# Performance work log

Measured on AMD Instinct MI355X. Metric: run time of the kernel, lower is better.

## Reference

```python
import jax, jax.numpy as jnp
import numpy as np

T, H, I, E, K = 4096, 2048, 1408, 8, 2


def setup_inputs() -> dict:
    key = jax.random.key(0)
    k1, k2, k3, k4, k5 = jax.random.split(key, 5)
    hidden_states = jax.random.normal(k1, (T, H), dtype=jnp.float32)
    w13 = jax.random.normal(k2, (E, 2 * I, H), dtype=jnp.float32) * 0.02
    w2 = jax.random.normal(k3, (E, H, I), dtype=jnp.float32) * 0.02
    topk_ids = jax.random.randint(k4, (T, K), 0, E, dtype=jnp.int32)
    topk_weights = jax.random.uniform(k5, (T, K), dtype=jnp.float32)
    return {
        "hidden_states": hidden_states,
        "w13": w13,
        "w2": w2,
        "topk_ids": topk_ids,
        "topk_weights": topk_weights,
    }


def reference(hidden_states, w13, w2, topk_ids, topk_weights):
    # hidden_states: [T, H]; w13: [E, 2I, H]; w2: [E, H, I]
    # topk_ids/topk_weights: [T, K]. local_expert_start = 0.
    num_tokens, hidden = hidden_states.shape
    num_experts = w13.shape[0]
    inter = w13.shape[1] // 2
    gate_w = w13[:, :inter, :]  # [E, I, H]
    up_w = w13[:, inter:, :]    # [E, I, H]

    # Dense per-expert gate/up projections (vectorized grouped GEMM).
    gate = jnp.einsum('th,eih->tei', hidden_states, gate_w)
    up = jnp.einsum('th,eih->tei', hidden_states, up_w)
    act = jax.nn.silu(gate) * up  # [T, E, I]

    # Scatter topk weights into a dense [T, E] routing matrix (zero elsewhere),
    # which reproduces the trivial impl's per-slot weighted accumulation.
    tok = jnp.arange(num_tokens, dtype=jnp.int32)[:, None]
    routing = jnp.zeros((num_tokens, num_experts), dtype=hidden_states.dtype)
    routing = routing.at[tok, topk_ids].add(topk_weights)

    # Weighted combine through the down projection; weighting act first avoids
    # materializing a [T, E, H] intermediate.
    act_w = act * routing[:, :, None]  # [T, E, I]
    out = jnp.einsum('tei,ehi->th', act_w, w2)  # [T, H]
    return out
```

## Files before the change

### kernel.cpp

```cpp
#include <hip/hip_runtime.h>
#include <hip/hip_bf16.h>

#define T_TOK 4096
#define HID   2048
#define INTER 1408
#define TWO_I 2816
#define NEXP  8
#define ROWCAP 9216

#define N8_HS  1048576
#define N8_W13 5767168
#define NCVT   ((N8_HS + N8_W13) / 256)

using bf16x8 = __attribute__((ext_vector_type(8))) __bf16;
using f32x4  = __attribute__((ext_vector_type(4))) float;

__device__ __forceinline__ unsigned short f2bf(float f) {
  unsigned u = __float_as_uint(f);
  u += 0x7fffu + ((u >> 16) & 1u);
  return (unsigned short)(u >> 16);
}

__device__ __forceinline__ void gload16(const void* g, void* l) {
  __builtin_amdgcn_global_load_lds(
      (const __attribute__((address_space(1))) void*)g,
      (__attribute__((address_space(3))) void*)l, 16, 0, 0);
}

__device__ __forceinline__ uint4 pack8(float4 a, float4 b) {
  union { unsigned short us[8]; uint4 v; } o;
  o.us[0] = f2bf(a.x); o.us[1] = f2bf(a.y); o.us[2] = f2bf(a.z); o.us[3] = f2bf(a.w);
  o.us[4] = f2bf(b.x); o.us[5] = f2bf(b.y); o.us[6] = f2bf(b.z); o.us[7] = f2bf(b.w);
  return o.v;
}

__global__ void cvt2route_kernel(const float* __restrict__ hs_f, unsigned short* __restrict__ hs_b,
                                 const float* __restrict__ w13_f, unsigned short* __restrict__ w13_b,
                                 const int* __restrict__ ids, const float* __restrict__ wts,
                                 float* __restrict__ R, int* __restrict__ counts) {
  int bid = blockIdx.x;
  if (bid >= NCVT) {
    int t = (bid - NCVT) * 256 + threadIdx.x;
    if (t >= T_TOK) return;
    int e0 = ids[t * 2], e1 = ids[t * 2 + 1];
    float w0 = wts[t * 2], w1 = wts[t * 2 + 1];
#pragma unroll
    for (int ee = 0; ee < NEXP; ++ee) {
      float r = (e0 == ee ? w0 : 0.0f) + (e1 == ee ? w1 : 0.0f);
      R[t * NEXP + ee] = r;
    }
    atomicAdd(&counts[e0], 1);
    if (e1 != e0) atomicAdd(&counts[e1], 1);
    return;
  }
  int i = bid * 256 + threadIdx.x;
  const float4* p;
  uint4* o;
  int j;
  if (i < N8_HS) {
    p = reinterpret_cast<const float4*>(hs_f);
    o = reinterpret_cast<uint4*>(hs_b);
    j = i;
  } else {
    p = reinterpret_cast<const float4*>(w13_f);
    o = reinterpret_cast<uint4*>(w13_b);
    j = i - N8_HS;
  }
  o[j] = pack8(p[j * 2], p[j * 2 + 1]);
}

__global__ void offsets_kernel(const int* __restrict__ counts,
                               int* __restrict__ offs, int* __restrict__ cursor,
                               int* __restrict__ tl) {
  if (threadIdx.x == 0) {
    int o = 0;
    for (int e = 0; e < NEXP; ++e) {
      offs[e] = o;
      cursor[e] = o;
      o += (counts[e] + 127) & ~127;
    }
    offs[NEXP] = o;
  }
  for (int i = threadIdx.x; i < ROWCAP; i += 256) tl[i] = -1;
}

__global__ void scatter_kernel(const int* __restrict__ ids,
                               int* __restrict__ cursor, int* __restrict__ tl,
                               int* __restrict__ inv) {
  int t = blockIdx.x * 256 + threadIdx.x;
  if (t >= T_TOK) return;
  int e0 = ids[t * 2], e1 = ids[t * 2 + 1];
  int p = atomicAdd(&cursor[e0], 1);
  tl[p] = t;
  inv[t * 2] = p;
  if (e1 != e0) {
    p = atomicAdd(&cursor[e1], 1);
    tl[p] = t;
    inv[t * 2 + 1] = p;
  } else {
    inv[t * 2 + 1] = -1;
  }
}


#define BARR do { __asm__ __volatile__("" ::: "memory"); \
                  __builtin_amdgcn_s_barrier();           \
                  __asm__ __volatile__("" ::: "memory"); } while (0)
#define VMC(n) __asm__ __volatile__("s_waitcnt vmcnt(" #n ")" ::: "memory")

#define STG(P, h, kt, slotOff, hOff)                                        \
  do {                                                                      \
    gload16(P[h][0] + (kt) * 128, smem + (slotOff) + (hOff) + chA);         \
    gload16(P[h][1] + (kt) * 128, smem + (slotOff) + (hOff) + chA + 1024);  \
  } while (0)

#define LDA(dst, S, aq)                                                     \
  do {                                                                      \
    _Pragma("unroll") for (int mi = 0; mi < 4; ++mi) {                      \
      const char* _p = smem + (S) + wmOff + ((aq) * 64 + mi * 16 + l15) * 128; \
      dst[mi][0] = *(const bf16x8*)(_p + ko0);                              \
      dst[mi][1] = *(const bf16x8*)(_p + ko1);                              \
    }                                                                       \
  } while (0)

#define LDB(dst, S, bq)                                                     \
  do {                                                                      \
    _Pragma("unroll") for (int ni = 0; ni < 2; ++ni) {                      \
      const char* _p = smem + (S) + 32768 + wnhOff +                        \
                       (wn1 * 64 + ((bq) * 2 + ni) * 16 + l15) * 128;       \
      dst[ni][0] = *(const bf16x8*)(_p + ko0);                              \
      dst[ni][1] = *(const bf16x8*)(_p + ko1);                              \
    }                                                                       \
  } while (0)

#define MFQ(A, B, aq, bq)                                                   \
  do {                                                                      \
    __builtin_amdgcn_s_setprio(1);                                          \
    _Pragma("unroll") for (int mi = 0; mi < 4; ++mi)                        \
    _Pragma("unroll") for (int ni = 0; ni < 2; ++ni) {                      \
      acc[(aq) * 4 + mi][(bq) * 2 + ni] = __builtin_amdgcn_mfma_f32_16x16x32_bf16( \
          A[mi][0], B[ni][0], acc[(aq) * 4 + mi][(bq) * 2 + ni], 0, 0, 0);  \
      acc[(aq) * 4 + mi][(bq) * 2 + ni] = __builtin_amdgcn_mfma_f32_16x16x32_bf16( \
          A[mi][1], B[ni][1], acc[(aq) * 4 + mi][(bq) * 2 + ni], 0, 0, 0);  \
    }                                                                       \
    __builtin_amdgcn_s_setprio(0);                                          \
  } while (0)

#define EIGHT_PHASES(NIT_, NL_LIM_)                                         \
  for (int i = 0; i < (NIT_); ++i) {                                        \
    const int t0 = 2 * i, t1 = t0 + 1;                                      \
    const bool nl = (i < (NL_LIM_));                                        \
                               \
    LDA(a_lo, 0, 0);                                                        \
    LDA(a_hi, 0, 1);                                                        \
    LDB(b_lo, 0, 0);                                                        \
    LDB(b_hi, 0, 1);                                                        \
    STG(aS, 0, t1, 65536, 0);                                               \
    BARR; MFQ(a_lo, b_lo, 0, 0); BARR;                                      \
                                                                    \
    STG(aS, 1, t1, 65536, 16384);                                           \
    BARR; MFQ(a_lo, b_hi, 0, 1); BARR;                                      \
                                                                    \
    if (nl) STG(bS, 0, t0 + 2, 0, 32768);                                   \
    BARR; MFQ(a_hi, b_hi, 1, 1); BARR;                                      \
                                                                    \
    if (nl) STG(bS, 1, t0 + 2, 0, 49152);                                   \
    BARR; MFQ(a_hi, b_lo, 1, 0);                                            \
    if (nl) { VMC(4); } else { VMC(0); }                                    \
    BARR;                                                                   \
                               \
    LDA(a_lo, 65536, 0);                                                    \
    LDA(a_hi, 65536, 1);                                                    \
    LDB(b_lo, 65536, 0);                                                    \
    LDB(b_hi, 65536, 1);                                                    \
    if (nl) STG(aS, 0, t0 + 2, 0, 0);                                       \
    BARR; MFQ(a_lo, b_lo, 0, 0); BARR;                                      \
                                                                    \
    if (nl) STG(aS, 1, t0 + 2, 0, 16384);                                   \
    BARR; MFQ(a_lo, b_hi, 0, 1); BARR;                                      \
                                                                    \
    if (nl) STG(bS, 0, t1 + 2, 65536, 32768);                               \
    BARR; MFQ(a_hi, b_hi, 1, 1); BARR;                                      \
                                                                    \
    if (nl) STG(bS, 1, t1 + 2, 65536, 49152);                               \
    BARR; MFQ(a_hi, b_lo, 1, 0);                                            \
    if (nl) VMC(4);                                                         \
    BARR;                                                                   \
  }

#define PROLOGUE_STAGE()                                                    \
  do {                                                                      \
    STG(aS, 0, 0, 0, 0);                                                    \
    STG(aS, 1, 0, 0, 16384);                                                \
    STG(bS, 0, 0, 0, 32768);                                                \
    STG(bS, 1, 0, 0, 49152);                                                \
    STG(bS, 0, 1, 65536, 32768);                                            \
    STG(bS, 1, 1, 65536, 49152);                                            \
    VMC(4);                                                                 \
    BARR;                                                                   \
  } while (0)

__global__ __launch_bounds__(512, 2) void gemm1_kernel(
    const unsigned short* __restrict__ hs,
    const unsigned short* __restrict__ w13,
    unsigned short* __restrict__ act,
    const int* __restrict__ tl, const int* __restrict__ offs,
    const float* __restrict__ w2f, unsigned short* __restrict__ w2b) {
  const int tid = threadIdx.x;
  const int lin = blockIdx.x + 11 * (blockIdx.y + 16 * blockIdx.z);

  {
    const float4* p = reinterpret_cast<const float4*>(w2f);
    uint4* o = reinterpret_cast<uint4*>(w2b);
    int gid = lin * 512 + tid;
#pragma unroll
    for (int q = 0; q < 4; ++q) {
      int idx = q * 720896 + gid;
      o[idx] = pack8(p[idx * 2], p[idx * 2 + 1]);
    }
  }

  const int work = (lin & 7) * 176 + (lin >> 3);
  const int bz = work / 176;
  const int rem = work - bz * 176;
  const int bx = rem % 11;
  const int by = rem / 11;

  const int e = bz;
  const int rbeg = offs[e], rend = offs[e + 1];
  const int m0 = rbeg + by * 256;
  if (m0 >= rend) return;
  const int n0 = bx * 128;

  __shared__ __align__(16) char smem[131072];

  const int lane = tid & 63, wave = tid >> 6;
  const int wm = wave >> 2, wn = wave & 3;
  const int l15 = lane & 15;
  const int srow = lane >> 3;
  const int scolswz = ((lane & 7) * 16) ^ (srow << 4);
  const int chA = wave * 2048;
  const int wmOff = wm * 16384;
  const int wnhOff = (wn >> 1) * 16384;
  const int wn1 = wn & 1;
  const int rsw = (lane & 7) << 4;
  const int ko0 = ((lane >> 4) * 16) ^ rsw;
  const int ko1 = (64 + (lane >> 4) * 16) ^ rsw;

  const char* hs_b = (const char*)hs;
  const char* w13_b = (const char*)w13 + (size_t)e * (TWO_I * HID * 2);

  const char* aS[2][2];
  const char* bS[2][2];
#pragma unroll
  for (int h = 0; h < 2; ++h)
#pragma unroll
    for (int it = 0; it < 2; ++it) {
      int rl = h * 128 + (wave * 2 + it) * 8 + srow;
      int grow = m0 + rl;
      int tk = (grow < rend) ? tl[grow] : 0;
      if (tk < 0) tk = 0;
      aS[h][it] = hs_b + (size_t)tk * 4096 + scolswz;
      int wg = rl >> 6, sub = rl & 63;
      int srcB = (sub < 32) ? (n0 + wg * 32 + sub)
                            : (INTER + n0 + wg * 32 + (sub - 32));
      bS[h][it] = w13_b + (size_t)srcB * 4096 + scolswz;
    }

  f32x4 acc[8][4] = {};
  bf16x8 a_lo[4][2], a_hi[4][2], b_lo[2][2], b_hi[2][2];

  PROLOGUE_STAGE();
  EIGHT_PHASES(16, 15);

  const bool okst = (wm == 0) || (rend - m0 >= 256);
  if (okst) {
#pragma unroll
    for (int MI = 0; MI < 8; ++MI)
#pragma unroll
      for (int j = 0; j < 4; ++j) {
        int row = m0 + wm * 128 + MI * 16 + (lane >> 4) * 4 + j;
        size_t base = (size_t)row * INTER + n0 + wn * 32;
#pragma unroll
        for (int NI = 0; NI < 2; ++NI) {
          float g = acc[MI][NI][j], u = acc[MI][NI + 2][j];
          float s = (g / (1.0f + __expf(-g))) * u;
          act[base + NI * 16 + l15] = f2bf(s);
        }
      }
  }
}

__global__ __launch_bounds__(512, 2) void gemm2_kernel(
    const unsigned short* __restrict__ act,
    const unsigned short* __restrict__ w2,
    const float* __restrict__ R, const int* __restrict__ tl,
    const int* __restrict__ offs, unsigned short* __restrict__ partial) {
  const int tid = threadIdx.x;
  const int lin = blockIdx.x + 8 * (blockIdx.y + 16 * blockIdx.z);
  const int work = (lin & 7) * 128 + (lin >> 3);
  const int bz = work >> 7;
  const int rem = work & 127;
  const int bx = rem & 7;
  const int by = rem >> 3;

  const int e = bz;
  const int rbeg = offs[e], rend = offs[e + 1];
  const int m0 = rbeg + by * 256;
  if (m0 >= rend) return;
  const int n0 = bx * 256;

  __shared__ __align__(16) char smem[131072];

  const int lane = tid & 63, wave = tid >> 6;
  const int wm = wave >> 2, wn = wave & 3;
  const int l15 = lane & 15;
  const int srow = lane >> 3;
  const int scolswz = ((lane & 7) * 16) ^ (srow << 4);
  const int chA = wave * 2048;
  const int wmOff = wm * 16384;
  const int wnhOff = (wn >> 1) * 16384;
  const int wn1 = wn & 1;
  const int rsw = (lane & 7) << 4;
  const int ko0 = ((lane >> 4) * 16) ^ rsw;
  const int ko1 = (64 + (lane >> 4) * 16) ^ rsw;

  const char* act_b = (const char*)act;
  const char* w2_b = (const char*)w2 + (size_t)e * (HID * INTER * 2);

  const char* aS[2][2];
  const char* bS[2][2];
#pragma unroll
  for (int h = 0; h < 2; ++h)
#pragma unroll
    for (int it = 0; it < 2; ++it) {
      int rl = h * 128 + (wave * 2 + it) * 8 + srow;
      int grow = m0 + rl;
      if (grow >= rend) grow = rbeg;
      aS[h][it] = act_b + (size_t)grow * (INTER * 2) + scolswz;
      bS[h][it] = w2_b + (size_t)(n0 + rl) * (INTER * 2) + scolswz;
    }

  f32x4 acc[8][4] = {};
  bf16x8 a_lo[4][2], a_hi[4][2], b_lo[2][2], b_hi[2][2];

  PROLOGUE_STAGE();
  EIGHT_PHASES(11, 10);

  const bool okst = (wm == 0) || (rend - m0 >= 256);
  if (okst) {
#pragma unroll
    for (int MI = 0; MI < 8; ++MI) {
      float sc[4];
#pragma unroll
      for (int j = 0; j < 4; ++j) {
        int row = m0 + wm * 128 + MI * 16 + (lane >> 4) * 4 + j;
        int t = tl[row];
        sc[j] = t >= 0 ? R[t * NEXP + e] : 0.0f;
      }
#pragma unroll
      for (int NI = 0; NI < 4; ++NI) {
        int col = n0 + wn * 64 + NI * 16 + l15;
#pragma unroll
        for (int j = 0; j < 4; ++j) {
          int row = m0 + wm * 128 + MI * 16 + (lane >> 4) * 4 + j;
          partial[(size_t)row * HID + col] = f2bf(acc[MI][NI][j] * sc[j]);
        }
      }
    }
  }
}

__global__ void combine_kernel(const unsigned short* __restrict__ P,
                               const int* __restrict__ inv,
                               float* __restrict__ out) {
  int idx = blockIdx.x * 256 + threadIdx.x;
  int t = idx >> 8;
  int c = (idx & 255) << 3;
  int p0 = inv[t * 2], p1 = inv[t * 2 + 1];
  union { uint4 v; unsigned short us[8]; } a, b;
  a.v = *(const uint4*)(P + (size_t)p0 * HID + c);
  float f[8];
#pragma unroll
  for (int j = 0; j < 8; ++j) f[j] = __uint_as_float((unsigned)a.us[j] << 16);
  if (p1 >= 0) {
    b.v = *(const uint4*)(P + (size_t)p1 * HID + c);
#pragma unroll
    for (int j = 0; j < 8; ++j) f[j] += __uint_as_float((unsigned)b.us[j] << 16);
  }
  float4 lo = {f[0], f[1], f[2], f[3]}, hi = {f[4], f[5], f[6], f[7]};
  *(float4*)(out + (size_t)t * HID + c) = lo;
  *(float4*)(out + (size_t)t * HID + c + 4) = hi;
}

extern "C" void kernel_launch(void* const* d_in, const int* in_sizes, int n_in,
                              void* d_out, int out_size, void* d_ws, size_t ws_size,
                              hipStream_t stream) {
  const float* hs_f  = (const float*)d_in[0];
  const float* w13_f = (const float*)d_in[1];
  const float* w2_f  = (const float*)d_in[2];
  const int*   ids   = (const int*)d_in[3];
  const float* wts   = (const float*)d_in[4];
  float* out = (float*)d_out;
  char* ws = (char*)d_ws;

  unsigned short* hs_b  = (unsigned short*)(ws);
  unsigned short* w13_b = (unsigned short*)(ws + 16777216);
  unsigned short* w2_b  = (unsigned short*)(ws + 109051904);
  unsigned short* act   = (unsigned short*)(ws + 155189248);
  float* R              = (float*)(ws + 181141504);
  int*   tl             = (int*)(ws + 181272576);
  int*   inv            = (int*)(ws + 181309440);
  int*   meta           = (int*)(ws + 181342208);
  unsigned short* partial = (unsigned short*)(ws + 16777216);
  int* counts = meta;
  int* offs   = meta + 8;
  int* cursor = meta + 17;

  hipMemsetAsync(meta, 0, 32 * sizeof(int), stream);

  cvt2route_kernel<<<dim3(NCVT + 16), dim3(256), 0, stream>>>(
      hs_f, hs_b, w13_f, w13_b, ids, wts, R, counts);

  offsets_kernel<<<dim3(1), dim3(256), 0, stream>>>(counts, offs, cursor, tl);
  scatter_kernel<<<dim3(T_TOK / 256), dim3(256), 0, stream>>>(ids, cursor, tl, inv);

  gemm1_kernel<<<dim3(11, 16, 8), dim3(512), 0, stream>>>(hs_b, w13_b, act, tl, offs, w2_f, w2_b);
  gemm2_kernel<<<dim3(8, 16, 8), dim3(512), 0, stream>>>(act, w2_b, R, tl, offs, partial);
  combine_kernel<<<dim3(T_TOK * (HID / 8) / 256), dim3(256), 0, stream>>>(partial, inv, out);
}
```

Before: 372.9 us.

## Fuse combine into gemm2 via float atomics and stagger LDS fragment loads

The down-projection kernel now scales each row by its routing weight and atomically adds it straight into the zeroed fp32 output. This removes the bf16 partial buffer and the separate combine kernel, at the cost of a full output memset and scattered fp32 atomics. The GEMM main loop also spreads the LDS fragment reads (b_hi, a_hi) across the MFMA phases so they are loaded closer to where they are used, which lowers register pressure and overlaps LDS reads with compute. A side effect is that results become nondeterministic in summation order, though partials are no longer rounded to bf16.

```diff
diff --git a/kernel.cpp b/kernel.cpp
--- a/kernel.cpp
+++ b/kernel.cpp
@@ -150,17 +150,17 @@
   for (int i = 0; i < (NIT_); ++i) {                                        \
     const int t0 = 2 * i, t1 = t0 + 1;                                      \
     const bool nl = (i < (NL_LIM_));                                        \
-                               \
+                                                                    \
     LDA(a_lo, 0, 0);                                                        \
-    LDA(a_hi, 0, 1);                                                        \
     LDB(b_lo, 0, 0);                                                        \
-    LDB(b_hi, 0, 1);                                                        \
     STG(aS, 0, t1, 65536, 0);                                               \
     BARR; MFQ(a_lo, b_lo, 0, 0); BARR;                                      \
                                                                     \
+    LDB(b_hi, 0, 1);                                                        \
     STG(aS, 1, t1, 65536, 16384);                                           \
     BARR; MFQ(a_lo, b_hi, 0, 1); BARR;                                      \
                                                                     \
+    LDA(a_hi, 0, 1);                                                        \
     if (nl) STG(bS, 0, t0 + 2, 0, 32768);                                   \
     BARR; MFQ(a_hi, b_hi, 1, 1); BARR;                                      \
                                                                     \
@@ -168,17 +168,17 @@
     BARR; MFQ(a_hi, b_lo, 1, 0);                                            \
     if (nl) { VMC(4); } else { VMC(0); }                                    \
     BARR;                                                                   \
-                               \
+                                                                    \
     LDA(a_lo, 65536, 0);                                                    \
-    LDA(a_hi, 65536, 1);                                                    \
     LDB(b_lo, 65536, 0);                                                    \
-    LDB(b_hi, 65536, 1);                                                    \
     if (nl) STG(aS, 0, t0 + 2, 0, 0);                                       \
     BARR; MFQ(a_lo, b_lo, 0, 0); BARR;                                      \
                                                                     \
+    LDB(b_hi, 65536, 1);                                                    \
     if (nl) STG(aS, 1, t0 + 2, 0, 16384);                                   \
     BARR; MFQ(a_lo, b_hi, 0, 1); BARR;                                      \
                                                                     \
+    LDA(a_hi, 65536, 1);                                                    \
     if (nl) STG(bS, 0, t1 + 2, 65536, 32768);                               \
     BARR; MFQ(a_hi, b_hi, 1, 1); BARR;                                      \
                                                                     \
@@ -295,7 +295,7 @@
     const unsigned short* __restrict__ act,
     const unsigned short* __restrict__ w2,
     const float* __restrict__ R, const int* __restrict__ tl,
-    const int* __restrict__ offs, unsigned short* __restrict__ partial) {
+    const int* __restrict__ offs, float* __restrict__ out) {
   const int tid = threadIdx.x;
   const int lin = blockIdx.x + 8 * (blockIdx.y + 16 * blockIdx.z);
   const int work = (lin & 7) * 128 + (lin >> 3);
@@ -351,11 +351,13 @@
   if (okst) {
 #pragma unroll
     for (int MI = 0; MI < 8; ++MI) {
+      int tt[4];
       float sc[4];
 #pragma unroll
       for (int j = 0; j < 4; ++j) {
         int row = m0 + wm * 128 + MI * 16 + (lane >> 4) * 4 + j;
         int t = tl[row];
+        tt[j] = t;
         sc[j] = t >= 0 ? R[t * NEXP + e] : 0.0f;
       }
 #pragma unroll
@@ -363,34 +365,12 @@
         int col = n0 + wn * 64 + NI * 16 + l15;
 #pragma unroll
         for (int j = 0; j < 4; ++j) {
-          int row = m0 + wm * 128 + MI * 16 + (lane >> 4) * 4 + j;
-          partial[(size_t)row * HID + col] = f2bf(acc[MI][NI][j] * sc[j]);
+          if (tt[j] >= 0)
+            atomicAdd(&out[(size_t)tt[j] * HID + col], acc[MI][NI][j] * sc[j]);
         }
       }
     }
   }
-}
-
-__global__ void combine_kernel(const unsigned short* __restrict__ P,
-                               const int* __restrict__ inv,
-                               float* __restrict__ out) {
-  int idx = blockIdx.x * 256 + threadIdx.x;
-  int t = idx >> 8;
-  int c = (idx & 255) << 3;
-  int p0 = inv[t * 2], p1 = inv[t * 2 + 1];
-  union { uint4 v; unsigned short us[8]; } a, b;
-  a.v = *(const uint4*)(P + (size_t)p0 * HID + c);
-  float f[8];
-#pragma unroll
-  for (int j = 0; j < 8; ++j) f[j] = __uint_as_float((unsigned)a.us[j] << 16);
-  if (p1 >= 0) {
-    b.v = *(const uint4*)(P + (size_t)p1 * HID + c);
-#pragma unroll
-    for (int j = 0; j < 8; ++j) f[j] += __uint_as_float((unsigned)b.us[j] << 16);
-  }
-  float4 lo = {f[0], f[1], f[2], f[3]}, hi = {f[4], f[5], f[6], f[7]};
-  *(float4*)(out + (size_t)t * HID + c) = lo;
-  *(float4*)(out + (size_t)t * HID + c + 4) = hi;
 }
 
 extern "C" void kernel_launch(void* const* d_in, const int* in_sizes, int n_in,
@@ -412,12 +392,12 @@
   int*   tl             = (int*)(ws + 181272576);
   int*   inv            = (int*)(ws + 181309440);
   int*   meta           = (int*)(ws + 181342208);
-  unsigned short* partial = (unsigned short*)(ws + 16777216);
   int* counts = meta;
   int* offs   = meta + 8;
   int* cursor = meta + 17;
 
   hipMemsetAsync(meta, 0, 32 * sizeof(int), stream);
+  hipMemsetAsync(out, 0, (size_t)T_TOK * HID * sizeof(float), stream);
 
   cvt2route_kernel<<<dim3(NCVT + 16), dim3(256), 0, stream>>>(
       hs_f, hs_b, w13_f, w13_b, ids, wts, R, counts);
@@ -426,6 +406,5 @@
   scatter_kernel<<<dim3(T_TOK / 256), dim3(256), 0, stream>>>(ids, cursor, tl, inv);
 
   gemm1_kernel<<<dim3(11, 16, 8), dim3(512), 0, stream>>>(hs_b, w13_b, act, tl, offs, w2_f, w2_b);
-  gemm2_kernel<<<dim3(8, 16, 8), dim3(512), 0, stream>>>(act, w2_b, R, tl, offs, partial);
-  combine_kernel<<<dim3(T_TOK * (HID / 8) / 256), dim3(256), 0, stream>>>(partial, inv, out);
-}
+  gemm2_kernel<<<dim3(8, 16, 8), dim3(512), 0, stream>>>(act, w2_b, R, tl, offs, out);
+}
```

Measured after the change: 331.2 us. 1.13x faster.
